# Optimization experiments

Measured on AMD Instinct MI355X. Metric: run time of the kernel, lower is better.

## Reference

```python
import jax, jax.numpy as jnp
import numpy as np

B, H, D, V = 1024, 4, 256, 100000


def setup_inputs() -> dict:
    key = jax.random.key(0)
    k1, k2, k3, k4 = jax.random.split(key, 4)
    x = jax.random.normal(k1, (B, D), dtype=jnp.float32)
    # Glorot-normal-ish scaling for the learned matrices
    proj_mat = jax.random.normal(k2, (H * D, D), dtype=jnp.float32) * (2.0 / (H * D + D)) ** 0.5
    mix_mat = jax.random.normal(k3, (H, D), dtype=jnp.float32) * (2.0 / (H + D)) ** 0.5
    emb = jax.random.normal(k4, (V, D), dtype=jnp.float32) * 0.05
    return {"x": x, "proj_mat": proj_mat, "mix_mat": mix_mat, "emb": emb}


def reference(x, proj_mat, mix_mat, emb):
    # per-head projection: [B, H*D] -> [B, H, D]
    proj = jnp.tanh(x @ proj_mat.T).reshape(B, H, D)
    # mixture weights over heads: [B, H]
    pi = jax.nn.softmax(x @ mix_mat.T, axis=-1)
    # full-vocab logits per head: [B, H, V]
    head_logits = jnp.einsum("bhd,vd->bhv", proj, emb)
    head_probs = jax.nn.softmax(head_logits, axis=-1)
    # weighted mixture over heads -> [B, V]
    probs = jnp.einsum("bh,bhv->bv", pi, head_probs)
    return probs
```

## Files before the change

### kernel.cpp

```cpp
#include <hip/hip_runtime.h>
#include <stdint.h>


#define VOCAB 100000
#define NVT 1564
#define VPAD 100096

typedef __attribute__((ext_vector_type(8))) short short8;
typedef __attribute__((ext_vector_type(4))) float f32x4;

__device__ __forceinline__ short f2bf(float f) {
  uint32_t u = __float_as_uint(f);
  u = (u + 0x7FFFu + ((u >> 16) & 1u)) >> 16;
  return (short)u;
}

__global__ __launch_bounds__(256) void proj_kernel(const float* __restrict__ x,
                                                   const float* __restrict__ pm,
                                                   short* __restrict__ projF) {
  __shared__ float xs[64][36];
  __shared__ float ps[64][36];
  const int tid = threadIdx.x;
  const int tx = tid & 15, ty = tid >> 4;
  const int m0 = blockIdx.y * 64, n0 = blockIdx.x * 64;
  float acc[4][4];
#pragma unroll
  for (int i = 0; i < 4; i++)
#pragma unroll
    for (int j = 0; j < 4; j++) acc[i][j] = 0.f;

  for (int k0 = 0; k0 < 256; k0 += 32) {
    const int r = tid >> 2, c = (tid & 3) * 8;
    *(float4*)&xs[r][c]     = *(const float4*)&x[(m0 + r) * 256 + k0 + c];
    *(float4*)&xs[r][c + 4] = *(const float4*)&x[(m0 + r) * 256 + k0 + c + 4];
    *(float4*)&ps[r][c]     = *(const float4*)&pm[(n0 + r) * 256 + k0 + c];
    *(float4*)&ps[r][c + 4] = *(const float4*)&pm[(n0 + r) * 256 + k0 + c + 4];
    __syncthreads();
#pragma unroll
    for (int kk = 0; kk < 32; kk += 4) {
      float4 xa[4], pb[4];
#pragma unroll
      for (int i = 0; i < 4; i++) xa[i] = *(const float4*)&xs[ty * 4 + i][kk];
#pragma unroll
      for (int j = 0; j < 4; j++) pb[j] = *(const float4*)&ps[tx * 4 + j][kk];
#pragma unroll
      for (int i = 0; i < 4; i++)
#pragma unroll
        for (int j = 0; j < 4; j++)
          acc[i][j] += xa[i].x * pb[j].x + xa[i].y * pb[j].y +
                       xa[i].z * pb[j].z + xa[i].w * pb[j].w;
    }
    __syncthreads();
  }
#pragma unroll
  for (int i = 0; i < 4; i++)
#pragma unroll
    for (int j = 0; j < 4; j++) {
      int b = m0 + ty * 4 + i, c = n0 + tx * 4 + j;
      int m = b * 4 + (c >> 8), k = c & 255;
      size_t addr = ((((size_t)(m >> 6) * 8 + (k >> 5)) * 4 + ((m >> 4) & 3)) * 64 +
                     ((k >> 3) & 3) * 16 + (m & 15)) * 8 + (k & 7);
      projF[addr] = f2bf(tanhf(acc[i][j]));
    }
}

__global__ __launch_bounds__(256) void pi_kernel(const float* __restrict__ x,
                                                 const float* __restrict__ mm,
                                                 float* __restrict__ pi) {
  int b = blockIdx.x * 256 + threadIdx.x;
  if (b >= 1024) return;
  float acc[4] = {0.f, 0.f, 0.f, 0.f};
  for (int k = 0; k < 256; k += 4) {
    float4 xv = *(const float4*)&x[(size_t)b * 256 + k];
#pragma unroll
    for (int h = 0; h < 4; h++) {
      float4 mv = *(const float4*)&mm[h * 256 + k];
      acc[h] += xv.x * mv.x + xv.y * mv.y + xv.z * mv.z + xv.w * mv.w;
    }
  }
  float mx = fmaxf(fmaxf(acc[0], acc[1]), fmaxf(acc[2], acc[3]));
  float e[4], ssum = 0.f;
#pragma unroll
  for (int h = 0; h < 4; h++) { e[h] = __expf(acc[h] - mx); ssum += e[h]; }
#pragma unroll
  for (int h = 0; h < 4; h++) pi[b * 4 + h] = e[h] / ssum;
}

__global__ __launch_bounds__(256) void embB_kernel(const float* __restrict__ emb,
                                                   short* __restrict__ embB) {
  size_t i = ((size_t)blockIdx.x * 256 + threadIdx.x) * 8;
  size_t row = i >> 8;
  const float C = 1.44269504088896f;
  short8 b8;
  if (row < VOCAB) {
    float4 f0 = *(const float4*)&emb[i];
    float4 f1 = *(const float4*)&emb[i + 4];
    b8[0] = f2bf(f0.x * C); b8[1] = f2bf(f0.y * C); b8[2] = f2bf(f0.z * C); b8[3] = f2bf(f0.w * C);
    b8[4] = f2bf(f1.x * C); b8[5] = f2bf(f1.y * C); b8[6] = f2bf(f1.z * C); b8[7] = f2bf(f1.w * C);
  } else {
#pragma unroll
    for (int j = 0; j < 8; ++j) b8[j] = 0;
  }
  *(short8*)&embB[i] = b8;
}


#define MFMA16(AF, KT)                                                                    \
  __builtin_amdgcn_s_setprio(1);                                                          \
  _Pragma("unroll") for (int mi = 0; mi < 4; ++mi)                                        \
      _Pragma("unroll") for (int ni = 0; ni < 4; ++ni)                                    \
          acc[mi][ni] = __builtin_amdgcn_mfma_f32_16x16x32_bf16(AF[mi], Bf[ni][KT],       \
                                                                acc[mi][ni], 0, 0, 0);    \
  __builtin_amdgcn_s_setprio(0);

template <int MODE>
__global__ __launch_bounds__(256, 2) void mos_gemm(const short* __restrict__ projF,
                                                   const short* __restrict__ embB_s,
                                                   const float* __restrict__ w,
                                                   float* __restrict__ part,
                                                   float* __restrict__ out) {
  const int tid = threadIdx.x;
  const int lane = tid & 63, wid = tid >> 6;
  const int l15 = lane & 15, l4 = lane >> 4;

  const int bid = blockIdx.x;
  const int xcd = bid & 7, idx = bid >> 3;
  const int vt = (xcd < 4) ? (xcd * 196 + idx) : (784 + (xcd - 4) * 195 + idx);
  const int v0 = vt * 64;
  const int M0 = wid * 1024;

  const int mts = (wid * 4 + idx) & 15;

  short8 Bf[4][8];
  {
    const short* bbase = embB_s + (size_t)(v0 + l15) * 256 + l4 * 8;
#pragma unroll
    for (int ni = 0; ni < 4; ++ni)
#pragma unroll
      for (int kt = 0; kt < 8; ++kt)
        Bf[ni][kt] = *(const short8*)(bbase + ni * 4096 + kt * 32);
  }

  f32x4 acc[4][4];
#pragma unroll
  for (int i = 0; i < 4; ++i)
#pragma unroll
    for (int j = 0; j < 4; ++j) acc[i][j] = (f32x4){0.f, 0.f, 0.f, 0.f};

  const short* aq = projF + (size_t)(M0 >> 6) * 32 * 512 + lane * 8;

  const short* ap = aq + mts * 16384;
  short8 aA[4], aB[4];
#pragma unroll
  for (int mi = 0; mi < 4; ++mi) aA[mi] = *(const short8*)(ap + mi * 512);

#pragma unroll 1
  for (int it = 0; it < 16; ++it) {
    const int mt = (mts + it) & 15;
    ap = aq + mt * 16384;
#pragma unroll
    for (int kt = 0; kt < 8; kt += 2) {
#pragma unroll
      for (int mi = 0; mi < 4; ++mi)
        aB[mi] = *(const short8*)(ap + (kt + 1) * 2048 + mi * 512);
      MFMA16(aA, kt);
#pragma unroll
      for (int mi = 0; mi < 4; ++mi)
        aA[mi] = *(const short8*)(ap + (kt + 2) * 2048 + mi * 512);
      MFMA16(aB, kt + 1);
    }
    if (mt == 15 && it < 15) {
#pragma unroll
      for (int mi = 0; mi < 4; ++mi) aA[mi] = *(const short8*)(aq + mi * 512);
    }

    if (MODE == 0) {
#pragma unroll
      for (int mi = 0; mi < 4; ++mi) {
        float p[4] = {0.f, 0.f, 0.f, 0.f};
#pragma unroll
        for (int ni = 0; ni < 4; ++ni) {
          int v = v0 + ni * 16 + l15;
          bool ok = v < VOCAB;
#pragma unroll
          for (int r = 0; r < 4; ++r) {
            float e = exp2f(acc[mi][ni][r]);
            p[r] += ok ? e : 0.f;
          }
          acc[mi][ni] = (f32x4){0.f, 0.f, 0.f, 0.f};
        }
#pragma unroll
        for (int r = 0; r < 4; ++r) {
          p[r] += __shfl_xor(p[r], 1, 64);
          p[r] += __shfl_xor(p[r], 2, 64);
          p[r] += __shfl_xor(p[r], 4, 64);
          p[r] += __shfl_xor(p[r], 8, 64);
        }
        if (l15 == 0) {
          int m = M0 + mt * 64 + mi * 16 + l4 * 4;
          float4 pv = {p[0], p[1], p[2], p[3]};
          *(float4*)(part + (size_t)vt * 4096 + m) = pv;
        }
      }
    } else {
#pragma unroll
      for (int mi = 0; mi < 4; ++mi) {
        int mrow = M0 + mt * 64 + mi * 16 + l4 * 4;
        float4 wv = *(const float4*)&w[mrow];
        size_t brow = (size_t)(mrow >> 2);
#pragma unroll
        for (int ni = 0; ni < 4; ++ni) {
          int v = v0 + ni * 16 + l15;
          float val = wv.x * exp2f(acc[mi][ni][0]) + wv.y * exp2f(acc[mi][ni][1]) +
                      wv.z * exp2f(acc[mi][ni][2]) + wv.w * exp2f(acc[mi][ni][3]);
          if (v < VOCAB) out[brow * VOCAB + v] = val;
          acc[mi][ni] = (f32x4){0.f, 0.f, 0.f, 0.f};
        }
      }
    }
  }
}

__global__ __launch_bounds__(256) void reduce_w(const float* __restrict__ part,
                                                const float* __restrict__ pi,
                                                float* __restrict__ w) {
  int m = blockIdx.x * 256 + threadIdx.x;
  float sum = 0.f;
  for (int c = 0; c < NVT; ++c) sum += part[(size_t)c * 4096 + m];
  w[m] = pi[m] / sum;
}

extern "C" void kernel_launch(void* const* d_in, const int* in_sizes, int n_in,
                              void* d_out, int out_size, void* d_ws, size_t ws_size,
                              hipStream_t stream) {
  const float* x        = (const float*)d_in[0];
  const float* proj_mat = (const float*)d_in[1];
  const float* mix_mat  = (const float*)d_in[2];
  const float* emb      = (const float*)d_in[3];
  float* out = (float*)d_out;

  char* ws = (char*)d_ws;
  short* projF = (short*)ws;
  float* pi    = (float*)(ws + (2u << 20));
  float* w     = (float*)(ws + (2u << 20) + 16384);
  short* embB  = (short*)(ws + (4u << 20));
  float* part  = (float*)(ws + (4u << 20) + (size_t)VPAD * 512);

  dim3 g1(16, 16);
  proj_kernel<<<g1, 256, 0, stream>>>(x, proj_mat, projF);
  pi_kernel<<<4, 256, 0, stream>>>(x, mix_mat, pi);
  embB_kernel<<<VPAD / 8, 256, 0, stream>>>(emb, embB);

  mos_gemm<0><<<NVT, 256, 0, stream>>>(projF, embB, nullptr, part, nullptr);
  reduce_w<<<16, 256, 0, stream>>>(part, pi, w);
  mos_gemm<1><<<NVT, 256, 0, stream>>>(projF, embB, w, nullptr, out);
}
```

Measured before the change: 705.5 us.

## Stream B tiles through 4-deep register ring instead of holding all B fragments

The embedding matrix is pre-swizzled into an MFMA-fragment-major layout so each wave reads contiguous per-lane chunks. The GEMM no longer keeps all 32 B fragments resident in registers. Instead it prefetches A and B fragments together three k-steps ahead through a 4-slot register ring, crossing m-tile boundaries. This cuts register pressure and tightens load/MFMA overlap, but B is now re-read from cache for every m-tile, which adds memory traffic.

```diff
diff --git a/kernel.cpp b/kernel.cpp
--- a/kernel.cpp
+++ b/kernel.cpp
@@ -86,36 +86,40 @@
   for (int h = 0; h < 4; h++) pi[b * 4 + h] = e[h] / ssum;
 }
 
-__global__ __launch_bounds__(256) void embB_kernel(const float* __restrict__ emb,
-                                                   short* __restrict__ embB) {
-  size_t i = ((size_t)blockIdx.x * 256 + threadIdx.x) * 8;
-  size_t row = i >> 8;
+__global__ __launch_bounds__(256) void embF_kernel(const float* __restrict__ emb,
+                                                   short* __restrict__ embF) {
+  int c8 = blockIdx.x * 256 + threadIdx.x;
+  int lane = c8 & 63, ni = (c8 >> 6) & 3, kt = (c8 >> 8) & 7, vt = c8 >> 11;
+  int v = vt * 64 + ni * 16 + (lane & 15);
+  int k = kt * 32 + ((lane >> 4) & 3) * 8;
   const float C = 1.44269504088896f;
   short8 b8;
-  if (row < VOCAB) {
-    float4 f0 = *(const float4*)&emb[i];
-    float4 f1 = *(const float4*)&emb[i + 4];
+  if (v < VOCAB) {
+    float4 f0 = *(const float4*)&emb[(size_t)v * 256 + k];
+    float4 f1 = *(const float4*)&emb[(size_t)v * 256 + k + 4];
     b8[0] = f2bf(f0.x * C); b8[1] = f2bf(f0.y * C); b8[2] = f2bf(f0.z * C); b8[3] = f2bf(f0.w * C);
     b8[4] = f2bf(f1.x * C); b8[5] = f2bf(f1.y * C); b8[6] = f2bf(f1.z * C); b8[7] = f2bf(f1.w * C);
   } else {
 #pragma unroll
     for (int j = 0; j < 8; ++j) b8[j] = 0;
   }
-  *(short8*)&embB[i] = b8;
-}
-
-
-#define MFMA16(AF, KT)                                                                    \
-  __builtin_amdgcn_s_setprio(1);                                                          \
-  _Pragma("unroll") for (int mi = 0; mi < 4; ++mi)                                        \
-      _Pragma("unroll") for (int ni = 0; ni < 4; ++ni)                                    \
-          acc[mi][ni] = __builtin_amdgcn_mfma_f32_16x16x32_bf16(AF[mi], Bf[ni][KT],       \
-                                                                acc[mi][ni], 0, 0, 0);    \
-  __builtin_amdgcn_s_setprio(0);
+  *(short8*)&embF[(size_t)c8 * 8] = b8;
+}
+
+
+#define LOADK(SLOT, MT, KT)                                                               \
+  do {                                                                                    \
+    const short* at_ = aq + (size_t)(((MT) * 8 + (KT)) * 4) * 512;                        \
+    const short* bt_ = bq + (KT) * 2048;                                                  \
+    _Pragma("unroll") for (int q = 0; q < 4; ++q)                                         \
+        ring[SLOT][q] = *(const short8*)(at_ + q * 512);                                  \
+    _Pragma("unroll") for (int q = 0; q < 4; ++q)                                         \
+        ring[SLOT][4 + q] = *(const short8*)(bt_ + q * 512);                              \
+  } while (0)
 
 template <int MODE>
 __global__ __launch_bounds__(256, 2) void mos_gemm(const short* __restrict__ projF,
-                                                   const short* __restrict__ embB_s,
+                                                   const short* __restrict__ embF,
                                                    const float* __restrict__ w,
                                                    float* __restrict__ part,
                                                    float* __restrict__ out) {
@@ -128,50 +132,41 @@
   const int vt = (xcd < 4) ? (xcd * 196 + idx) : (784 + (xcd - 4) * 195 + idx);
   const int v0 = vt * 64;
   const int M0 = wid * 1024;
-
   const int mts = (wid * 4 + idx) & 15;
 
-  short8 Bf[4][8];
-  {
-    const short* bbase = embB_s + (size_t)(v0 + l15) * 256 + l4 * 8;
-#pragma unroll
-    for (int ni = 0; ni < 4; ++ni)
-#pragma unroll
-      for (int kt = 0; kt < 8; ++kt)
-        Bf[ni][kt] = *(const short8*)(bbase + ni * 4096 + kt * 32);
-  }
-
+  const short* aq = projF + (size_t)(M0 >> 6) * 32 * 512 + lane * 8;
+  const short* bq = embF + (size_t)vt * 16384 + lane * 8;
+
+  short8 ring[4][8];
   f32x4 acc[4][4];
 #pragma unroll
   for (int i = 0; i < 4; ++i)
 #pragma unroll
     for (int j = 0; j < 4; ++j) acc[i][j] = (f32x4){0.f, 0.f, 0.f, 0.f};
 
-  const short* aq = projF + (size_t)(M0 >> 6) * 32 * 512 + lane * 8;
-
-  const short* ap = aq + mts * 16384;
-  short8 aA[4], aB[4];
-#pragma unroll
-  for (int mi = 0; mi < 4; ++mi) aA[mi] = *(const short8*)(ap + mi * 512);
+  LOADK(0, mts, 0);
+  LOADK(1, mts, 1);
+  LOADK(2, mts, 2);
 
 #pragma unroll 1
   for (int it = 0; it < 16; ++it) {
     const int mt = (mts + it) & 15;
-    ap = aq + mt * 16384;
-#pragma unroll
-    for (int kt = 0; kt < 8; kt += 2) {
+    const int mtn = (mts + it + 1) & 15;
+#pragma unroll
+    for (int kt = 0; kt < 8; ++kt) {
+      if (kt < 5) {
+        LOADK((kt + 3) & 3, mt, kt + 3);
+      } else if (it < 15) {
+        LOADK((kt + 3) & 3, mtn, kt - 5);
+      }
+      __builtin_amdgcn_s_setprio(1);
 #pragma unroll
       for (int mi = 0; mi < 4; ++mi)
-        aB[mi] = *(const short8*)(ap + (kt + 1) * 2048 + mi * 512);
-      MFMA16(aA, kt);
-#pragma unroll
-      for (int mi = 0; mi < 4; ++mi)
-        aA[mi] = *(const short8*)(ap + (kt + 2) * 2048 + mi * 512);
-      MFMA16(aB, kt + 1);
-    }
-    if (mt == 15 && it < 15) {
-#pragma unroll
-      for (int mi = 0; mi < 4; ++mi) aA[mi] = *(const short8*)(aq + mi * 512);
+#pragma unroll
+        for (int ni = 0; ni < 4; ++ni)
+          acc[mi][ni] = __builtin_amdgcn_mfma_f32_16x16x32_bf16(
+              ring[kt & 3][mi], ring[kt & 3][4 + ni], acc[mi][ni], 0, 0, 0);
+      __builtin_amdgcn_s_setprio(0);
     }
 
     if (MODE == 0) {
@@ -243,15 +238,15 @@
   short* projF = (short*)ws;
   float* pi    = (float*)(ws + (2u << 20));
   float* w     = (float*)(ws + (2u << 20) + 16384);
-  short* embB  = (short*)(ws + (4u << 20));
-  float* part  = (float*)(ws + (4u << 20) + (size_t)VPAD * 512);
+  short* embF  = (short*)(ws + (4u << 20));
+  float* part  = (float*)(ws + (4u << 20) + (size_t)NVT * 32768);
 
   dim3 g1(16, 16);
   proj_kernel<<<g1, 256, 0, stream>>>(x, proj_mat, projF);
   pi_kernel<<<4, 256, 0, stream>>>(x, mix_mat, pi);
-  embB_kernel<<<VPAD / 8, 256, 0, stream>>>(emb, embB);
-
-  mos_gemm<0><<<NVT, 256, 0, stream>>>(projF, embB, nullptr, part, nullptr);
+  embF_kernel<<<NVT * 16384 / 256 / 8, 256, 0, stream>>>(emb, embF);
+
+  mos_gemm<0><<<NVT, 256, 0, stream>>>(projF, embF, nullptr, part, nullptr);
   reduce_w<<<16, 256, 0, stream>>>(part, pi, w);
-  mos_gemm<1><<<NVT, 256, 0, stream>>>(projF, embB, w, nullptr, out);
-}
+  mos_gemm<1><<<NVT, 256, 0, stream>>>(projF, embF, w, nullptr, out);
+}
```

Measured after the change: 1.326 ms. +87.9%, slower.

## Cache fp16 head exponentials in first pass and mix them in a separate kernel

Applied to the files above, without the earlier changes.

The first GEMM pass now stores each computed exp2 value as fp16 into a large workspace buffer. A new elementwise mix kernel then combines those values with the per-row weights to produce the output, replacing the second full GEMM pass. This trades the recomputed matmul for roughly 1.6 GB of extra memory traffic and adds fp16 rounding of the probabilities. The new path is used only when the workspace is large enough; otherwise the original two-pass path runs.

```diff
diff --git a/kernel.cpp b/kernel.cpp
--- a/kernel.cpp
+++ b/kernel.cpp
@@ -1,10 +1,12 @@
 #include <hip/hip_runtime.h>
+#include <hip/hip_fp16.h>
 #include <stdint.h>
 
 
 #define VOCAB 100000
 #define NVT 1564
 #define VPAD 100096
+#define ETOT (((size_t)NVT) << 16)
 
 typedef __attribute__((ext_vector_type(8))) short short8;
 typedef __attribute__((ext_vector_type(4))) float f32x4;
@@ -13,6 +15,10 @@
   uint32_t u = __float_as_uint(f);
   u = (u + 0x7FFFu + ((u >> 16) & 1u)) >> 16;
   return (short)u;
+}
+__device__ __forceinline__ uint32_t pkh(float a, float b) {
+  __half2 h = __floats2half2_rn(a, b);
+  return *reinterpret_cast<uint32_t*>(&h);
 }
 
 __global__ __launch_bounds__(256) void proj_kernel(const float* __restrict__ x,
@@ -113,11 +119,12 @@
                                                                 acc[mi][ni], 0, 0, 0);    \
   __builtin_amdgcn_s_setprio(0);
 
-template <int MODE>
+template <int MODE, int EST>
 __global__ __launch_bounds__(256, 2) void mos_gemm(const short* __restrict__ projF,
                                                    const short* __restrict__ embB_s,
                                                    const float* __restrict__ w,
                                                    float* __restrict__ part,
+                                                   char* __restrict__ eF,
                                                    float* __restrict__ out) {
   const int tid = threadIdx.x;
   const int lane = tid & 63, wid = tid >> 6;
@@ -128,7 +135,6 @@
   const int vt = (xcd < 4) ? (xcd * 196 + idx) : (784 + (xcd - 4) * 195 + idx);
   const int v0 = vt * 64;
   const int M0 = wid * 1024;
-
   const int mts = (wid * 4 + idx) & 15;
 
   short8 Bf[4][8];
@@ -148,7 +154,6 @@
     for (int j = 0; j < 4; ++j) acc[i][j] = (f32x4){0.f, 0.f, 0.f, 0.f};
 
   const short* aq = projF + (size_t)(M0 >> 6) * 32 * 512 + lane * 8;
-
   const short* ap = aq + mts * 16384;
   short8 aA[4], aB[4];
 #pragma unroll
@@ -182,11 +187,16 @@
         for (int ni = 0; ni < 4; ++ni) {
           int v = v0 + ni * 16 + l15;
           bool ok = v < VOCAB;
-#pragma unroll
-          for (int r = 0; r < 4; ++r) {
-            float e = exp2f(acc[mi][ni][r]);
-            p[r] += ok ? e : 0.f;
+          float er[4];
+#pragma unroll
+          for (int r = 0; r < 4; ++r) er[r] = exp2f(acc[mi][ni][r]);
+          if (EST) {
+            size_t chunk = ((((size_t)vt * 4 + wid) * 16 + mt) * 4 + mi) * 4 + ni;
+            uint2 q = {pkh(er[0], er[1]), pkh(er[2], er[3])};
+            *(uint2*)(eF + chunk * 512 + lane * 8) = q;
           }
+#pragma unroll
+          for (int r = 0; r < 4; ++r) p[r] += ok ? er[r] : 0.f;
           acc[mi][ni] = (f32x4){0.f, 0.f, 0.f, 0.f};
         }
 #pragma unroll
@@ -228,6 +238,27 @@
   float sum = 0.f;
   for (int c = 0; c < NVT; ++c) sum += part[(size_t)c * 4096 + m];
   w[m] = pi[m] / sum;
+}
+
+__global__ __launch_bounds__(256) void mix_kernel(const char* __restrict__ eF,
+                                                  const float* __restrict__ w,
+                                                  float* __restrict__ out) {
+  const size_t stride = (size_t)gridDim.x * 256;
+  for (size_t u = (size_t)blockIdx.x * 256 + threadIdx.x; u < ETOT; u += stride) {
+    uint2 q = *(const uint2*)(eF + u * 8);
+    int lane = (int)(u & 63);
+    int ni = (int)((u >> 6) & 3), mi = (int)((u >> 8) & 3);
+    int mt = (int)((u >> 10) & 15), mq = (int)((u >> 14) & 3);
+    int vt = (int)(u >> 16);
+    int v = vt * 64 + ni * 16 + (lane & 15);
+    int b = mq * 256 + mt * 16 + mi * 4 + (lane >> 4);
+    __half2 h0 = *reinterpret_cast<__half2*>(&q.x);
+    __half2 h1 = *reinterpret_cast<__half2*>(&q.y);
+    float4 wv = *(const float4*)&w[b * 4];
+    float val = wv.x * __low2float(h0) + wv.y * __high2float(h0) +
+                wv.z * __low2float(h1) + wv.w * __high2float(h1);
+    if (v < VOCAB) out[(size_t)b * VOCAB + v] = val;
+  }
 }
 
 extern "C" void kernel_launch(void* const* d_in, const int* in_sizes, int n_in,
@@ -245,13 +276,21 @@
   float* w     = (float*)(ws + (2u << 20) + 16384);
   short* embB  = (short*)(ws + (4u << 20));
   float* part  = (float*)(ws + (4u << 20) + (size_t)VPAD * 512);
+  char*  eF    = ws + (88u << 20);
+  const size_t need = ((size_t)88 << 20) + ETOT * 8;
 
   dim3 g1(16, 16);
   proj_kernel<<<g1, 256, 0, stream>>>(x, proj_mat, projF);
   pi_kernel<<<4, 256, 0, stream>>>(x, mix_mat, pi);
   embB_kernel<<<VPAD / 8, 256, 0, stream>>>(emb, embB);
 
-  mos_gemm<0><<<NVT, 256, 0, stream>>>(projF, embB, nullptr, part, nullptr);
-  reduce_w<<<16, 256, 0, stream>>>(part, pi, w);
-  mos_gemm<1><<<NVT, 256, 0, stream>>>(projF, embB, w, nullptr, out);
-}
+  if (ws_size >= need) {
+    mos_gemm<0, 1><<<NVT, 256, 0, stream>>>(projF, embB, nullptr, part, eF, nullptr);
+    reduce_w<<<16, 256, 0, stream>>>(part, pi, w);
+    mix_kernel<<<4096, 256, 0, stream>>>(eF, w, out);
+  } else {
+    mos_gemm<0, 0><<<NVT, 256, 0, stream>>>(projF, embB, nullptr, part, nullptr, nullptr);
+    reduce_w<<<16, 256, 0, stream>>>(part, pi, w);
+    mos_gemm<1, 0><<<NVT, 256, 0, stream>>>(projF, embB, w, nullptr, nullptr, out);
+  }
+}
```

Result: slower. 796.1 us (+12.8%).
